# Optimization experiments

Hardware: AMD Instinct MI355X
Metric: run time of the kernel (lower is better)

The kernel has to match this reference:

```python
import jax, jax.numpy as jnp
import numpy as np

REG_COEF = 25.0


def _reflect(points, planes):
    # points: [B,P,3], planes: [B,4] -> reflected points [B,P,3]
    normals = planes[:, 0:3] / jnp.linalg.norm(planes[:, 0:3], axis=1, keepdims=True)
    offsets = planes[:, 3]
    # signed distance of each point to the plane: [B,P]
    dist = jnp.einsum('bd,bpd->bp', normals, points) + offsets[:, None]
    return points - 2.0 * dist[..., None] * normals[:, None, :]


def _chamfer(x, y):
    # x,y: [B,P,3]; pytorch3d chamfer_distance default:
    # mean over points, mean over batch, sum of both directions (squared dists)
    x2 = jnp.sum(x * x, axis=-1)  # [B,P]
    y2 = jnp.sum(y * y, axis=-1)  # [B,P]
    # pairwise squared distances [B,P,P]
    d = x2[:, :, None] + y2[:, None, :] - 2.0 * jnp.einsum('bpd,bqd->bpq', x, y)
    d = jnp.maximum(d, 0.0)
    cham_x = jnp.mean(jnp.min(d, axis=2))  # x -> nearest in y
    cham_y = jnp.mean(jnp.min(d, axis=1))  # y -> nearest in x
    return cham_x + cham_y


def _reg_loss(planes):
    # planes: [B,H,4]
    normals = planes[:, :, :3]
    normals = normals / jnp.linalg.norm(normals, axis=2, keepdims=True)
    H = normals.shape[1]
    a = jnp.einsum('bhd,bgd->bhg', normals, normals) - jnp.eye(H, dtype=normals.dtype)
    # Frobenius norm per batch -> [B]
    return jnp.sqrt(jnp.sum(a * a, axis=(1, 2)))


def setup_inputs() -> dict:
    key = jax.random.key(0)
    k1, k2 = jax.random.split(key)
    B, H, P = 8, 3, 4096
    return {
        'predicted_planes': jax.random.normal(k1, (B, H, 4), dtype=jnp.float32),
        'sample_points': jax.random.normal(k2, (B, P, 3), dtype=jnp.float32),
        'voxel_grids': jnp.zeros((B, 32, 32, 32), dtype=jnp.float32),
        'cp_grids': jnp.zeros((B, 32, 32, 32), dtype=jnp.float32),
    }


def reference(predicted_planes, sample_points, voxel_grids, cp_grids):
    n_heads = predicted_planes.shape[1]
    reg = jnp.sum(_reg_loss(predicted_planes))
    refl = jnp.asarray(0.0, dtype=sample_points.dtype)
    for h in range(n_heads):  # small fixed head count (3)
        reflected = _reflect(sample_points, predicted_planes[:, h, :])
        refl = refl + _chamfer(sample_points, reflected)
    return refl + REG_COEF * reg
```

## Files before the change

kernel.cpp:

```cpp
#include <hip/hip_runtime.h>
#include <math.h>

#define NB 8
#define NH 3
#define NBH 24
#define NP 4096
#define BLK 256
#define RPB 128
#define ROWBLKS (NP / RPB)
#define NPART (ROWBLKS * NBH)

typedef _Float16 half4 __attribute__((ext_vector_type(4)));
typedef _Float16 half8 __attribute__((ext_vector_type(8)));
typedef float floatx16 __attribute__((ext_vector_type(16)));

#define MIN3(r, a, b) asm("v_min3_f32 %0, %0, %1, %2" : "+v"(r) : "v"(a), "v"(b))

#define MFMA16Z(d, a, bb) \
    asm("v_mfma_f32_32x32x16_f16 %0, %1, %2, 0" : "=&v"(d) : "v"(a), "v"(bb))

__global__ void __launch_bounds__(BLK, 4) chamfer_mfma(const float* __restrict__ pts,
                                                       const float* __restrict__ planes,
                                                       float* __restrict__ partials) {
    __shared__ _Float16 qcols[NP * 4];
    __shared__ float bsum[4];

    const int tid  = threadIdx.x;
    const int lane = tid & 63;
    const int wave = tid >> 6;
    const int bh   = blockIdx.y;
    const int b    = bh / NH;
    const int h    = lane >> 5;

    const float* pl = planes + bh * 4;
    float n0 = pl[0], n1 = pl[1], n2 = pl[2], off = pl[3];
    float inv = 1.0f / sqrtf(n0 * n0 + n1 * n1 + n2 * n2);
    n0 *= inv; n1 *= inv; n2 *= inv;

    const float* bp = pts + (size_t)b * NP * 3;

    const int row = blockIdx.x * RPB + wave * 32 + (lane & 31);
    float a0 = bp[row * 3 + 0], a1 = bp[row * 3 + 1], a2 = bp[row * 3 + 2];

    #pragma unroll 4
    for (int i = tid; i < NP; i += BLK) {
        float y0 = bp[i * 3 + 0], y1 = bp[i * 3 + 1], y2 = bp[i * 3 + 2];
        float t = 2.0f * (n0 * y0 + n1 * y1 + n2 * y2 + off);
        y0 -= t * n0; y1 -= t * n1; y2 -= t * n2;
        float csq = y0 * y0 + y1 * y1 + y2 * y2;
        half4 q = { (_Float16)(-2.0f * y0), (_Float16)(-2.0f * y1),
                    (_Float16)(-2.0f * y2), (_Float16)csq };
        *(half4*)&qcols[i * 4] = q;
    }

    float rsqv = a0 * a0 + a1 * a1 + a2 * a2;
    half8 Aev = {0, 0, 0, 0, 0, 0, 0, 0};
    half8 Aod = {0, 0, 0, 0, 0, 0, 0, 0};
    if (lane < 32) {
        Aev[0] = (_Float16)a0; Aev[1] = (_Float16)a1;
        Aev[2] = (_Float16)a2; Aev[3] = (_Float16)1.0f;
        Aod[4] = (_Float16)a0; Aod[5] = (_Float16)a1;
        Aod[6] = (_Float16)a2; Aod[7] = (_Float16)1.0f;
    }
    __syncthreads();

    float rm[16];
    #pragma unroll
    for (int j = 0; j < 16; ++j) rm[j] = 1e30f;

    const _Float16* bcol = &qcols[(lane & 31) * 8];
    #define LD(u) (*(const half8*)(bcol + (u) * 256))

    half8 c0 = LD(0), c1 = LD(1), c2 = LD(2), c3 = LD(3);
    floatx16 dA0, dA1, dB0, dB1;
    MFMA16Z(dA0, Aev, c0);  MFMA16Z(dA1, Aod, c0);
    MFMA16Z(dB0, Aev, c1);  MFMA16Z(dB1, Aod, c1);

    #pragma unroll 1
    for (int u = 4; u <= 60; u += 4) {
        c0 = LD(u);
        #pragma unroll
        for (int j = 0; j < 16; ++j) MIN3(rm[j], dA0[j], dA1[j]);
        MFMA16Z(dA0, Aev, c2);  MFMA16Z(dA1, Aod, c2);
        c1 = LD(u + 1);
        #pragma unroll
        for (int j = 0; j < 16; ++j) MIN3(rm[j], dB0[j], dB1[j]);
        MFMA16Z(dB0, Aev, c3);  MFMA16Z(dB1, Aod, c3);
        c2 = LD(u + 2);
        #pragma unroll
        for (int j = 0; j < 16; ++j) MIN3(rm[j], dA0[j], dA1[j]);
        MFMA16Z(dA0, Aev, c0);  MFMA16Z(dA1, Aod, c0);
        c3 = LD(u + 3);
        #pragma unroll
        for (int j = 0; j < 16; ++j) MIN3(rm[j], dB0[j], dB1[j]);
        MFMA16Z(dB0, Aev, c1);  MFMA16Z(dB1, Aod, c1);
    }
    {
        #pragma unroll
        for (int j = 0; j < 16; ++j) MIN3(rm[j], dA0[j], dA1[j]);
        MFMA16Z(dA0, Aev, c2);  MFMA16Z(dA1, Aod, c2);
        #pragma unroll
        for (int j = 0; j < 16; ++j) MIN3(rm[j], dB0[j], dB1[j]);
        MFMA16Z(dB0, Aev, c3);  MFMA16Z(dB1, Aod, c3);
        #pragma unroll
        for (int j = 0; j < 16; ++j) MIN3(rm[j], dA0[j], dA1[j]);
        #pragma unroll
        for (int j = 0; j < 16; ++j) MIN3(rm[j], dB0[j], dB1[j]);
    }
    #undef LD

    #pragma unroll
    for (int j = 0; j < 16; ++j) {
        float v = rm[j];
        v = fminf(v, __shfl_xor(v, 1));
        v = fminf(v, __shfl_xor(v, 2));
        v = fminf(v, __shfl_xor(v, 4));
        v = fminf(v, __shfl_xor(v, 8));
        v = fminf(v, __shfl_xor(v, 16));
        rm[j] = v;
    }

    float s = 0.0f;
    #pragma unroll
    for (int j = 0; j < 16; ++j) {
        float rsqj = __shfl(rsqv, (j & 3) + 8 * (j >> 2) + 4 * h);
        s += fmaxf(rm[j] + rsqj, 0.0f);
    }
    s += __shfl_xor(s, 32);

    if (lane == 0) bsum[wave] = s;
    __syncthreads();
    if (tid == 0)
        partials[blockIdx.y * ROWBLKS + blockIdx.x] =
            bsum[0] + bsum[1] + bsum[2] + bsum[3];
}

__global__ void __launch_bounds__(256) finalize(const float* __restrict__ planes,
                                                const float* __restrict__ partials,
                                                float* __restrict__ out) {
    __shared__ float acc[4];
    const int tid = threadIdx.x;
    float s = partials[tid] + partials[tid + 256] + partials[tid + 512];
    #pragma unroll
    for (int o = 32; o; o >>= 1) s += __shfl_down(s, o);
    if ((tid & 63) == 0) acc[tid >> 6] = s;
    __syncthreads();
    if (tid == 0) {
        float cham = (acc[0] + acc[1] + acc[2] + acc[3]) * (2.0f / (float)(NB * NP));
        float reg = 0.0f;
        for (int bb = 0; bb < NB; ++bb) {
            float n[NH][3];
            for (int hh = 0; hh < NH; ++hh) {
                const float* p2 = planes + (bb * NH + hh) * 4;
                float a0 = p2[0], a1 = p2[1], a2 = p2[2];
                float iv = 1.0f / sqrtf(a0 * a0 + a1 * a1 + a2 * a2);
                n[hh][0] = a0 * iv; n[hh][1] = a1 * iv; n[hh][2] = a2 * iv;
            }
            float fro = 0.0f;
            for (int i = 0; i < NH; ++i)
                for (int j = 0; j < NH; ++j) {
                    float d = n[i][0] * n[j][0] + n[i][1] * n[j][1] + n[i][2] * n[j][2]
                              - (i == j ? 1.0f : 0.0f);
                    fro += d * d;
                }
            reg += 25.0f * sqrtf(fro);
        }
        out[0] = cham + reg;
    }
}

extern "C" void kernel_launch(void* const* d_in, const int* in_sizes, int n_in,
                              void* d_out, int out_size, void* d_ws, size_t ws_size,
                              hipStream_t stream) {
    const float* planes = (const float*)d_in[0];
    const float* pts    = (const float*)d_in[1];
    float* out          = (float*)d_out;
    float* partials     = (float*)d_ws;

    dim3 grid(ROWBLKS, NBH);
    chamfer_mfma<<<grid, BLK, 0, stream>>>(pts, planes, partials);
    finalize<<<1, 256, 0, stream>>>(planes, partials, out);
}
```

Measured before the change: 78.30 us.

## Split column range across two wave groups with shared-memory row-min merge

Doubles the block to 512 threads so the 4096 reflected columns are split between two groups of four waves, each scanning half the columns for the same 128 rows. Each wave now keeps a single MFMA accumulator chain instead of two interleaved ones. Per-row minima are merged through shared memory and the row sum is done by two waves. The finalize kernel also switches to double-precision accumulation. This gives more waves per CU and shorter per-wave serial loops, at the cost of an extra block barrier, shared-memory merge traffic and less independent MFMA work within each wave.

```diff
diff --git a/kernel.cpp b/kernel.cpp
--- a/kernel.cpp
+++ b/kernel.cpp
@@ -5,7 +5,7 @@
 #define NH 3
 #define NBH 24
 #define NP 4096
-#define BLK 256
+#define BLK 512
 #define RPB 128
 #define ROWBLKS (NP / RPB)
 #define NPART (ROWBLKS * NBH)
@@ -19,15 +19,19 @@
 #define MFMA16Z(d, a, bb) \
     asm("v_mfma_f32_32x32x16_f16 %0, %1, %2, 0" : "=&v"(d) : "v"(a), "v"(bb))
 
-__global__ void __launch_bounds__(BLK, 4) chamfer_mfma(const float* __restrict__ pts,
+__global__ void __launch_bounds__(BLK, 6) chamfer_mfma(const float* __restrict__ pts,
                                                        const float* __restrict__ planes,
                                                        float* __restrict__ partials) {
     __shared__ _Float16 qcols[NP * 4];
-    __shared__ float bsum[4];
+    __shared__ float rsqbuf[RPB];
+    __shared__ float rowmin[2][RPB];
+    __shared__ float bsum[2];
 
     const int tid  = threadIdx.x;
     const int lane = tid & 63;
     const int wave = tid >> 6;
+    const int rw   = wave & 3;
+    const int ch   = wave >> 2;
     const int bh   = blockIdx.y;
     const int b    = bh / NH;
     const int h    = lane >> 5;
@@ -39,7 +43,7 @@
 
     const float* bp = pts + (size_t)b * NP * 3;
 
-    const int row = blockIdx.x * RPB + wave * 32 + (lane & 31);
+    const int row = blockIdx.x * RPB + rw * 32 + (lane & 31);
     float a0 = bp[row * 3 + 0], a1 = bp[row * 3 + 1], a2 = bp[row * 3 + 2];
 
     #pragma unroll 4
@@ -62,6 +66,7 @@
         Aod[4] = (_Float16)a0; Aod[5] = (_Float16)a1;
         Aod[6] = (_Float16)a2; Aod[7] = (_Float16)1.0f;
     }
+    if (ch == 0 && lane < 32) rsqbuf[rw * 32 + (lane & 31)] = rsqv;
     __syncthreads();
 
     float rm[16];
@@ -69,43 +74,44 @@
     for (int j = 0; j < 16; ++j) rm[j] = 1e30f;
 
     const _Float16* bcol = &qcols[(lane & 31) * 8];
+    const int U0 = ch * 32;
     #define LD(u) (*(const half8*)(bcol + (u) * 256))
 
-    half8 c0 = LD(0), c1 = LD(1), c2 = LD(2), c3 = LD(3);
-    floatx16 dA0, dA1, dB0, dB1;
+    half8 c0 = LD(U0), c1 = LD(U0 + 1), c2 = LD(U0 + 2), c3 = LD(U0 + 3);
+    floatx16 dA0, dA1;
     MFMA16Z(dA0, Aev, c0);  MFMA16Z(dA1, Aod, c0);
-    MFMA16Z(dB0, Aev, c1);  MFMA16Z(dB1, Aod, c1);
 
     #pragma unroll 1
-    for (int u = 4; u <= 60; u += 4) {
-        c0 = LD(u);
+    for (int u = U0; u < U0 + 28; u += 4) {
+        c0 = LD(u + 4);
+        #pragma unroll
+        for (int j = 0; j < 16; ++j) MIN3(rm[j], dA0[j], dA1[j]);
+        MFMA16Z(dA0, Aev, c1);  MFMA16Z(dA1, Aod, c1);
+        c1 = LD(u + 5);
         #pragma unroll
         for (int j = 0; j < 16; ++j) MIN3(rm[j], dA0[j], dA1[j]);
         MFMA16Z(dA0, Aev, c2);  MFMA16Z(dA1, Aod, c2);
-        c1 = LD(u + 1);
+        c2 = LD(u + 6);
         #pragma unroll
-        for (int j = 0; j < 16; ++j) MIN3(rm[j], dB0[j], dB1[j]);
-        MFMA16Z(dB0, Aev, c3);  MFMA16Z(dB1, Aod, c3);
-        c2 = LD(u + 2);
+        for (int j = 0; j < 16; ++j) MIN3(rm[j], dA0[j], dA1[j]);
+        MFMA16Z(dA0, Aev, c3);  MFMA16Z(dA1, Aod, c3);
+        c3 = LD(u + 7);
         #pragma unroll
         for (int j = 0; j < 16; ++j) MIN3(rm[j], dA0[j], dA1[j]);
         MFMA16Z(dA0, Aev, c0);  MFMA16Z(dA1, Aod, c0);
-        c3 = LD(u + 3);
-        #pragma unroll
-        for (int j = 0; j < 16; ++j) MIN3(rm[j], dB0[j], dB1[j]);
-        MFMA16Z(dB0, Aev, c1);  MFMA16Z(dB1, Aod, c1);
     }
     {
         #pragma unroll
         for (int j = 0; j < 16; ++j) MIN3(rm[j], dA0[j], dA1[j]);
+        MFMA16Z(dA0, Aev, c1);  MFMA16Z(dA1, Aod, c1);
+        #pragma unroll
+        for (int j = 0; j < 16; ++j) MIN3(rm[j], dA0[j], dA1[j]);
         MFMA16Z(dA0, Aev, c2);  MFMA16Z(dA1, Aod, c2);
         #pragma unroll
-        for (int j = 0; j < 16; ++j) MIN3(rm[j], dB0[j], dB1[j]);
-        MFMA16Z(dB0, Aev, c3);  MFMA16Z(dB1, Aod, c3);
+        for (int j = 0; j < 16; ++j) MIN3(rm[j], dA0[j], dA1[j]);
+        MFMA16Z(dA0, Aev, c3);  MFMA16Z(dA1, Aod, c3);
         #pragma unroll
         for (int j = 0; j < 16; ++j) MIN3(rm[j], dA0[j], dA1[j]);
-        #pragma unroll
-        for (int j = 0; j < 16; ++j) MIN3(rm[j], dB0[j], dB1[j]);
     }
     #undef LD
 
@@ -120,33 +126,39 @@
         rm[j] = v;
     }
 
-    float s = 0.0f;
-    #pragma unroll
-    for (int j = 0; j < 16; ++j) {
-        float rsqj = __shfl(rsqv, (j & 3) + 8 * (j >> 2) + 4 * h);
-        s += fmaxf(rm[j] + rsqj, 0.0f);
+    if ((lane & 31) == 0) {
+        #pragma unroll
+        for (int j = 0; j < 16; ++j)
+            rowmin[ch][rw * 32 + (j & 3) + 8 * (j >> 2) + 4 * h] = rm[j];
     }
-    s += __shfl_xor(s, 32);
+    __syncthreads();
 
-    if (lane == 0) bsum[wave] = s;
+    if (tid < RPB) {
+        float m = fminf(rowmin[0][tid], rowmin[1][tid]);
+        float v = fmaxf(m + rsqbuf[tid], 0.0f);
+        #pragma unroll
+        for (int o = 32; o; o >>= 1) v += __shfl_down(v, o);
+        if ((tid & 63) == 0) bsum[tid >> 6] = v;
+    }
     __syncthreads();
     if (tid == 0)
-        partials[blockIdx.y * ROWBLKS + blockIdx.x] =
-            bsum[0] + bsum[1] + bsum[2] + bsum[3];
+        partials[blockIdx.y * ROWBLKS + blockIdx.x] = bsum[0] + bsum[1];
 }
 
 __global__ void __launch_bounds__(256) finalize(const float* __restrict__ planes,
                                                 const float* __restrict__ partials,
                                                 float* __restrict__ out) {
-    __shared__ float acc[4];
+    __shared__ double acc[4];
     const int tid = threadIdx.x;
-    float s = partials[tid] + partials[tid + 256] + partials[tid + 512];
+    double s = (double)partials[tid] + (double)partials[tid + 256]
+             + (double)partials[tid + 512];
     #pragma unroll
     for (int o = 32; o; o >>= 1) s += __shfl_down(s, o);
     if ((tid & 63) == 0) acc[tid >> 6] = s;
     __syncthreads();
     if (tid == 0) {
-        float cham = (acc[0] + acc[1] + acc[2] + acc[3]) * (2.0f / (float)(NB * NP));
+        double cham = (acc[0] + acc[1] + acc[2] + acc[3])
+                      * (2.0 / (double)(NB * NP));
         float reg = 0.0f;
         for (int bb = 0; bb < NB; ++bb) {
             float n[NH][3];
@@ -165,7 +177,7 @@
                 }
             reg += 25.0f * sqrtf(fro);
         }
-        out[0] = cham + reg;
+        out[0] = (float)cham + reg;
     }
 }
 
```

New measurement: 79.80 us. Within noise of the previous version (+1.9%).
